# Kernel tuning notes

Hardware: AMD Instinct MI355X
Metric: run time of the kernel (lower is better)

Reference implementation:

```python
import jax, jax.numpy as jnp
import numpy as np
import random as _pyrandom

# static config (must match init_kwargs)
LAYER_NODES = 2
NUM_LEVELS = 2
KERNEL = 3
STRIDE = 2
DILATION = 3
BN_EPS = 1e-5
B, T, C = 64, 4096, 64

# ---- static interleave-index builders (replace torch per-element cat loops with one gather) ----

def _joint_indices(a_len, b_len, node_idx):
    # Block.joint: interleave a (cur) with skip=2**(node_idx-1) elems of b (prev) per a-step.
    skip = 2 ** (node_idx - 1)
    idx, cnt = [], 0
    for i in range(a_len):
        for _ in range(skip):
            if cnt >= b_len:
                break
            idx.append(a_len + cnt)
            cnt += 1
        idx.append(i)
    return np.asarray(idx, np.int32)


def _joint_explict_indices(a_len, b_len, c_len):
    # Block.joint_explict: round-robin a,b,c then tails in order a,b,c.
    m = min(a_len, b_len, c_len)
    idx = []
    for t in range(m):
        idx += [t, a_len + t, a_len + b_len + t]
    idx += list(range(m, a_len))
    idx += list(range(a_len + m, a_len + b_len))
    idx += list(range(a_len + b_len + m, a_len + b_len + c_len))
    return np.asarray(idx, np.int32)


def _dpadding_indices(a_len, num_padding):
    # Block.dpadding: duplicate every skip_cnt-th element until num_padding extras inserted.
    if num_padding == 0:
        return np.arange(a_len, dtype=np.int32)
    target = a_len + num_padding
    skip_cnt = a_len // num_padding
    mult = None
    if skip_cnt == 0:
        mult = num_padding // a_len
        skip_cnt = 1
    entries = []  # list-of-lists mimics torch list entries (slab counts as 1 entry, as in source)
    rem = num_padding
    for i in range(a_len):
        if rem == 0:
            entries.append(list(range(i, a_len)))
            break
        if i % skip_cnt == 0:
            entries.append([i])
            rem -= 1
        if mult is not None:
            entries.extend([[i]] * mult)
        entries.append([i])
    if len(entries) > target:  # randrange pop path; deterministic seed (never hit for these shapes)
        rng = _pyrandom.Random(0)
        for _ in range(len(entries) - target):
            entries.pop(rng.randrange(len(entries)))
    return np.asarray([k for e in entries for k in e], np.int32)


def _sew_up_indices(a_len, b_len, cur_layer, sp, st):
    # Block.sew_up for cur_layer > 0; st carries the mutable skip_* counters.
    idx = []
    cnt_a = cnt_b = 0
    while cnt_a < a_len:
        if sp:
            break
        if cnt_a == 0:
            pv = cnt_b  # prev_val captured once in torch source
            for _ in range(st['skip_p']):
                idx.append(a_len + pv)
                cnt_b += 1
            if cur_layer % 2 != 0:
                idx.append(0)
                cnt_a += 1
            if cnt_a == 0:
                cnt_a = 1
            continue
        for _ in range(st['skip_n']):
            if cnt_b >= b_len:
                break
            idx.append(a_len + cnt_b)
            cnt_b += 1
        if not st['skip_t']:
            for _ in range(st['skip_s']):
                if cnt_b >= b_len:
                    break
                idx.append(a_len + cnt_b)
                cnt_b += 1
                st['skip_t'] = True
        else:
            for _j in range(st['skip_d']):
                for _i in range(st['skip_s']):
                    if cnt_b >= b_len:
                        break
                    idx.append(a_len + cnt_b)
                    cnt_b += 1
                if cnt_a >= a_len:
                    break
                idx.append(cnt_a)
                cnt_a += 1
                st['skip_t'] = False
            continue
        idx.append(cnt_a)
        cnt_a += 1
    idx += [a_len + j for j in range(cnt_b, b_len)]
    if sp:
        idx += list(range(cnt_a, a_len))
    st['skip_s'] += 1
    st['skip_n'] = 3 * st['skip_n'] + st['skip_s'] + st['skip_d'] * st['skip_s']
    if cur_layer % 2 != 0:
        st['skip_p'] += 1
    return np.asarray(idx, np.int32)

# ---- jax compute blocks ----

def _conv_block(y, v, g, b):
    # weight_norm(Conv1d): w = g * v / ||v||_(in,k) per out-channel; then MaxPool1d(3,2,pad=1), ELU (dropout=0)
    nrm = jnp.sqrt(jnp.sum(v * v, axis=(1, 2), keepdims=True))
    w = (g[:, None, None] / nrm) * v
    y = jax.lax.conv_general_dilated(y, w, (STRIDE,), 'VALID', rhs_dilation=(DILATION,),
                                     dimension_numbers=('NCH', 'OIH', 'NCH'))
    y = y + b[None, :, None]
    y = jax.lax.reduce_window(y, -jnp.inf, jax.lax.max, (1, 1, KERNEL), (1, 1, STRIDE),
                              ((0, 0), (0, 0), (1, 1)))
    return jax.nn.elu(y)


def _batchnorm(y, gamma, beta):
    # BatchNorm1d training-mode batch stats (biased var), per channel over (N, L)
    mu = jnp.mean(y, axis=(0, 2), keepdims=True)
    var = jnp.mean((y - mu) ** 2, axis=(0, 2), keepdims=True)
    return gamma[None, :, None] * (y - mu) * jax.lax.rsqrt(var + BN_EPS) + beta[None, :, None]


def _communicate(xn, prev_out, node_idx, mean, std, conv_v, conv_g, conv_b, bn_gamma, bn_beta):
    if node_idx == 0:
        return xn
    while prev_out.shape[2] != xn.shape[2]:  # static-shape loop
        prev_out = jnp.diff(prev_out, axis=2)
    out_mean = 0.8 * xn / mean + 0.2 * prev_out
    out_std = 0.8 * xn / std + 0.2 * prev_out
    L = xn.shape[2]
    je = _joint_explict_indices(L, L, L)
    joined = jnp.concatenate([out_mean, prev_out, out_std], axis=2)[:, :, je]
    y = jnp.exp(_conv_block(joined, conv_v, conv_g, conv_b) ** 2 / -2)
    pad_idx = _dpadding_indices(y.shape[2], L - y.shape[2])
    y = y[:, :, pad_idx]
    y = _batchnorm(y, bn_gamma, bn_beta)
    y = jax.nn.elu(y)  # Dropout(0.1) in eval -> identity
    return xn + y


def _forward(x, conv_v, conv_g, conv_b, bn_gamma, bn_beta):
    x = jnp.transpose(x, (0, 2, 1))  # [B, C, T]
    mean = jnp.mean(x)
    std = jnp.std(x, ddof=1)  # torch.std is unbiased
    # Graph.build_graph: level l node (l*LAYER_NODES + i) = x strided by LAYER_NODES, l+1 times
    nodes = {}
    for i in range(LAYER_NODES):
        cur = x
        for lvl in range(NUM_LEVELS):
            cur = cur[:, :, i::LAYER_NODES]
            assert cur.shape[2] >= 10, 'sp stat-padding path not exercised with these shapes'
            nodes[lvl * LAYER_NODES + i] = cur
    st = dict(skip_p=1, skip_s=1, skip_d=2, skip_n=3, skip_t=False)
    prev_layer_out = None
    cur_layer_out = None
    for i in range(NUM_LEVELS):
        cur_layer_out = None
        prev_out = None
        for j in range(LAYER_NODES + 1):
            cur_node = i * LAYER_NODES if j == LAYER_NODES else j + i * LAYER_NODES
            node_idx = j % LAYER_NODES
            out = _communicate(nodes[cur_node], prev_out, node_idx, mean, std,
                               conv_v, conv_g, conv_b, bn_gamma, bn_beta)
            prev_out = out
            if cur_layer_out is None:
                cur_layer_out = out
            if node_idx != 0:
                ji = _joint_indices(prev_out.shape[2], cur_layer_out.shape[2], node_idx)
                cur_layer_out = jnp.concatenate([prev_out, cur_layer_out], axis=2)[:, :, ji]
            if j == LAYER_NODES and i > 0:  # sew_up is identity at level 0
                si = _sew_up_indices(cur_layer_out.shape[2], prev_layer_out.shape[2], i, False, st)
                cur_layer_out = jnp.concatenate([cur_layer_out, prev_layer_out], axis=2)[:, :, si]
        prev_layer_out = cur_layer_out
    return cur_layer_out  # [B, C, 6144]


def setup_inputs() -> dict:
    key = jax.random.key(0)
    k1, k2, k3 = jax.random.split(key, 3)
    return {
        'x': jax.random.normal(k1, (B, T, C), dtype=jnp.float32),
        'conv_v': jax.random.normal(k2, (C, C, KERNEL), dtype=jnp.float32) * 0.1,
        'conv_g': jax.random.uniform(k3, (C,), dtype=jnp.float32) + 0.5,
        'conv_b': jnp.zeros((C,), jnp.float32),
        'bn_gamma': jnp.ones((C,), jnp.float32),
        'bn_beta': jnp.zeros((C,), jnp.float32),
    }


def reference(x, conv_v, conv_g, conv_b, bn_gamma, bn_beta):
    return _forward(x, conv_v, conv_g, conv_b, bn_gamma, bn_beta)
```

## Files before the change

### kernel.cpp

```cpp
#include <hip/hip_runtime.h>
#include <math.h>

#define BB 64
#define TT 4096
#define CC 64

constexpr int L0v = 2048, U0v = 3069, V0v = 1535, P0v = 2048;
constexpr int L1v = 1024, U1v = 1533, V1v = 767,  P1v = 1024;
constexpr int OUTL = 6144;
constexpr long NTOT = (long)BB * TT * CC;
#define VB 30
#define NB0 52
#define NB1 26
#define NTILE ((NB0 + NB1) * 64)
#define SRTOT 87
#define RSTR 65
#define EROWS 63

__global__ __launch_bounds__(256) void transpose_stats(const float* __restrict__ x,
                                                       float* __restrict__ xtr,
                                                       double* __restrict__ part) {
  __shared__ float tile[64][65];
  __shared__ double sd1[256], sd2[256];
  const int tt = blockIdx.x;
  const int b = blockIdx.y;
  const int t0 = tt * 64;
  const long xbase = (long)b * TT * CC + (long)t0 * CC;
  const int tid = threadIdx.x;
  double a = 0, q = 0;
  {
    int c = tid & 63;
    for (int r = tid >> 6; r < 64; r += 4) {
      float v = x[xbase + r * 64 + c];
      tile[r][c] = v;
      a += v; q += (double)v * (double)v;
    }
  }
  sd1[tid] = a; sd2[tid] = q;
  __syncthreads();
  {
    int tl = tid & 63;
    for (int cc = tid >> 6; cc < 64; cc += 4)
      xtr[((long)(b * 64 + cc)) * TT + t0 + tl] = tile[tl][cc];
  }
  for (int s = 128; s > 0; s >>= 1) {
    if (tid < s) { sd1[tid] += sd1[tid + s]; sd2[tid] += sd2[tid + s]; }
    __syncthreads();
  }
  if (tid == 0) {
    part[(b * 64 + tt) * 2] = sd1[0];
    part[(b * 64 + tt) * 2 + 1] = sd2[0];
  }
}

__device__ __host__ inline int pad_idx(int p, int brk, int dup, int sub) {
  if (p < brk) { int q = p / 3; int r = p - 3 * q; return 2 * q + (r == 2 ? 1 : 0); }
  if (p < brk + 2) return dup;
  return p - sub;
}

__device__ inline int fmap_code(int k) {
  if (k == 0) return 2048 + 0;
  if (k == 1) return 0;
  if (k < 5462) {
    int m = k - 2;
    int c = m / 12;
    int j = m - 12 * c;
    if (j <= 3)  return 2048 + (1 + 9 * c + j);
    if (j == 4)  return 1 + 3 * c;
    if (j <= 8)  return 2048 + (9 * c + j);
    if (j == 9)  return 2 + 3 * c;
    if (j == 10) return 2048 + (9 + 9 * c);
    return 3 + 3 * c;
  }
  return k - 4096;
}

__global__ __launch_bounds__(256) void prep(const double* __restrict__ part,
                                            double* __restrict__ stats,
                                            const float* __restrict__ v,
                                            const float* __restrict__ g,
                                            float* __restrict__ wt,
                                            int* __restrict__ codes) {
  const int blk = blockIdx.x;
  const int tid = threadIdx.x;
  if (blk == 0) {
    __shared__ double s1[256], s2[256];
    double a = 0, q = 0;
    for (int i = tid; i < 4096; i += 256) { a += part[2 * i]; q += part[2 * i + 1]; }
    s1[tid] = a; s2[tid] = q;
    __syncthreads();
    for (int s = 128; s > 0; s >>= 1) {
      if (tid < s) { s1[tid] += s1[tid + s]; s2[tid] += s2[tid + s]; }
      __syncthreads();
    }
    if (tid == 0) {
      double n = (double)NTOT;
      double mean = s1[0] / n;
      double var = (s2[0] - s1[0] * s1[0] / n) / (n - 1.0);
      stats[0] = mean; stats[1] = sqrt(var);
      stats[2] = 0.8 / mean;
      stats[3] = 0.8 / sqrt(var);
    }
  } else if (blk <= 64) {
    int o = blk - 1;
    __shared__ float red[256];
    __shared__ float scale;
    float vv = (tid < 192) ? v[o * 192 + tid] : 0.f;
    red[tid] = vv * vv;
    __syncthreads();
    for (int s = 128; s > 0; s >>= 1) {
      if (tid < s) red[tid] += red[tid + s];
      __syncthreads();
    }
    if (tid == 0) scale = g[o] / sqrtf(red[0]);
    __syncthreads();
    if (tid < 192) {
      int i = tid / 3, k = tid - 3 * i;
      wt[(k * 64 + i) * 64 + o] = scale * vv;
    }
  } else {
    int k = (blk - 65) * 256 + tid;
    if (k < OUTL) {
      int s = fmap_code(k);
      int type, xi, yi = 0;
      if (s < 2048) {
        if ((s & 1) == 0) { type = 0; xi = 2 * s; }
        else { int p = s >> 1; yi = pad_idx(p, 768, 512, 257); xi = 4 * p + 3; type = 2; }
      } else {
        int p = s - 2048;
        if ((p & 1) == 0) { type = 0; xi = p; }
        else { int q = p >> 1; yi = pad_idx(q, 1536, 1024, 513); xi = 2 * q + 1; type = 1; }
      }
      codes[k] = type | (xi << 2) | (yi << 14);
    }
  }
}

__global__ __launch_bounds__(256, 7) void conv_pool(
    const float* __restrict__ x, const float* __restrict__ wt,
    const float* __restrict__ cbias, const double* __restrict__ stats,
    float* __restrict__ y10, float* __restrict__ y11,
    float* __restrict__ part) {
  const int b = blockIdx.x;
  const int jb = blockIdx.y;
  const bool lev0 = jb < NB0;
  const int v0 = (lev0 ? jb : jb - NB0) * VB;
  const int L = lev0 ? L0v : L1v;
  const int U = lev0 ? U0v : U1v;
  const int V = lev0 ? V0v : V1v;
  const int mult = lev0 ? 2 : 4;
  const int off1 = lev0 ? 1 : 3;
  const int mid = lev0 ? 1024 : 512;
  float* __restrict__ y1 = lev0 ? y10 : y11;

  const int tid = threadIdx.x;
  const int lane = tid & 63;
  const int og = __builtin_amdgcn_readfirstlane((tid >> 6) * 16);

  const int a0 = (v0 == 0) ? 0 : (2 * v0 - 1) / 3;

  __shared__ __align__(16) float S[SRTOT * RSTR];
  float* cbf = S;
  float* red = S + 4096;

  const float ivm = (float)stats[2];
  const float ivs = (float)stats[3];
  const long xbase = (long)b * TT * CC;

  for (int idx = tid; idx < SRTOT * 16; idx += 256) {
    int d = idx >> 4, c4 = (idx & 15) * 4;
    int T = (d < 44) ? (2 * a0 + d) : (2 * a0 + d - 44);
    int Tc = min(max(T, 0), L - 1);
    long row = (long)(mult * Tc) * CC + ((d < 44) ? 0 : off1) * CC;
    float4 vr = *(const float4*)&x[xbase + row + c4];
    float* dst = S + d * RSTR + c4;
    dst[0] = vr.x; dst[1] = vr.y; dst[2] = vr.z; dst[3] = vr.w;
  }
  __syncthreads();

  const int rho = (lane <= 41) ? lane : ((lane == 63) ? 0 : (44 + 2 * (lane - 42)));
  const float* Sx = S + rho * RSTR;

  float acc[16];
#pragma unroll
  for (int oo = 0; oo < 16; oo++) acc[oo] = 0.f;

  for (int k = 0; k < 3; k++) {
    const float* Sk = Sx + k * RSTR;
    const float* wk = wt + (k * 64) * 64 + og;
#pragma unroll 4
    for (int i4 = 0; i4 < 16; i4++) {
      float x0 = Sk[i4 * 4 + 0];
      float x1 = Sk[i4 * 4 + 1];
      float x2 = Sk[i4 * 4 + 2];
      float x3 = Sk[i4 * 4 + 3];
      const float* wp = wk + i4 * 256;
#pragma unroll
      for (int oo = 0; oo < 16; oo++) {
        float w0 = wp[oo], w1 = wp[64 + oo], w2 = wp[128 + oo], w3 = wp[192 + oo];
        acc[oo] = fmaf(x0, w0, acc[oo]);
        acc[oo] = fmaf(x1, w1, acc[oo]);
        acc[oo] = fmaf(x2, w2, acc[oo]);
        acc[oo] = fmaf(x3, w3, acc[oo]);
      }
    }
  }

  __syncthreads();
  if (lane < EROWS) {
#pragma unroll
    for (int oo = 0; oo < 16; oo++)
      cbf[lane * RSTR + og + oo] = acc[oo];
  }
  __syncthreads();

  const int o = tid >> 2;
  const float bias = cbias[o];
  float a1 = 0.f, a2 = 0.f;
  for (int vq = tid & 3; vq < VB; vq += 4) {
    int v = v0 + vq;
    if (v < V) {
      float m3 = -INFINITY;
#pragma unroll
      for (int p = 0; p < 3; p++) {
        int u = 2 * v - 1 + p;
        float mv = -INFINITY;
        if (u >= 0 && u < U) {
          int a = u / 3;
          int r = u - 3 * a;
          int ai = a - a0;
          if (r == 2) {
            mv = cbf[(2 * ai + 1) * RSTR + o] + bias;
          } else {
            float e1 = cbf[(42 + ai) * RSTR + o];
            float e0 = cbf[(2 * ai) * RSTR + o];
            mv = fmaf(r ? ivs : ivm, e1, fmaf(0.2f, e0, bias));
          }
        }
        m3 = fmaxf(m3, mv);
      }
      float e = (m3 > 0.f) ? m3 : (expf(m3) - 1.f);
      float y = expf(-0.5f * e * e);
      y1[(long)(b * 64 + o) * V + v] = y;
      float wv = (v < mid) ? (float)(2 - (v & 1)) : ((v == mid) ? 2.f : 1.f);
      a1 += wv * y;
      a2 += wv * y * y;
    }
  }
  red[o * 4 + (tid & 3)] = a1;
  red[256 + o * 4 + (tid & 3)] = a2;
  __syncthreads();
  if (tid < 64) {
    float s1 = red[tid * 4] + red[tid * 4 + 1] + red[tid * 4 + 2] + red[tid * 4 + 3];
    float s2 = red[256 + tid * 4] + red[256 + tid * 4 + 1] + red[256 + tid * 4 + 2] + red[256 + tid * 4 + 3];
    long tile = (long)jb * 64 + b;
    part[tile * 128 + tid * 2] = s1;
    part[tile * 128 + tid * 2 + 1] = s2;
  }
}

__global__ __launch_bounds__(256) void bn_reduce(const float* __restrict__ part,
                                                 const float* __restrict__ gamma,
                                                 const float* __restrict__ beta,
                                                 float* __restrict__ cf0,
                                                 float* __restrict__ cf1) {
  const int bc = blockIdx.x;
  const int lev = bc >> 6, c = bc & 63;
  const long t_lo = lev ? (long)NB0 * 64 : 0;
  const long t_hi = lev ? (long)(NB0 + NB1) * 64 : (long)NB0 * 64;
  const int tid = threadIdx.x;
  double a = 0, q = 0;
  for (long t = t_lo + tid; t < t_hi; t += 256) {
    a += part[t * 128 + c * 2];
    q += part[t * 128 + c * 2 + 1];
  }
  __shared__ double s1[256], s2[256];
  s1[tid] = a; s2[tid] = q;
  __syncthreads();
  for (int s = 128; s > 0; s >>= 1) {
    if (tid < s) { s1[tid] += s1[tid + s]; s2[tid] += s2[tid + s]; }
    __syncthreads();
  }
  if (tid == 0) {
    double n = (double)BB * (lev ? P1v : P0v);
    double mu = s1[0] / n;
    double var = s2[0] / n - mu * mu;
    float rsig = 1.0f / sqrtf((float)var + 1e-5f);
    float A = gamma[c] * rsig;
    float Bv = beta[c] - (float)mu * A;
    float* cf = lev ? cf1 : cf0;
    cf[2 * c] = A;
    cf[2 * c + 1] = Bv;
  }
}

__global__ __launch_bounds__(256) void final_fused(
    const float* __restrict__ xtr, const float* __restrict__ y10,
    const float* __restrict__ y11, const float* __restrict__ cf0,
    const float* __restrict__ cf1, const int* __restrict__ codes,
    float* __restrict__ out) {
  const int bc = blockIdx.y;
  const int k = blockIdx.x * 256 + threadIdx.x;
  const int c = bc & 63;
  const float A0 = cf0[2 * c], B0 = cf0[2 * c + 1];
  const float A1 = cf1[2 * c], B1 = cf1[2 * c + 1];
  const float* xr  = xtr + (long)bc * TT;
  const float* y0r = y10 + (long)bc * V0v;
  const float* y1r = y11 + (long)bc * V1v;

  int code = codes[k];
  int type = code & 3;
  int xi = (code >> 2) & 4095;
  int yi = code >> 14;
  float xv = xr[xi];
  const float* yrow = (type == 2) ? y1r : y0r;
  float yv = yrow[yi];
  float A = (type == 0) ? 0.f : ((type == 2) ? A1 : A0);
  float Bv = (type == 0) ? 0.f : ((type == 2) ? B1 : B0);
  float z = fmaf(A, yv, Bv);
  float e = (z > 0.f) ? z : (expf(z) - 1.f);
  out[(long)bc * OUTL + k] = xv + e;
}

extern "C" void kernel_launch(void* const* d_in, const int* in_sizes, int n_in,
                              void* d_out, int out_size, void* d_ws, size_t ws_size,
                              hipStream_t stream) {
  const float* x   = (const float*)d_in[0];
  const float* cv  = (const float*)d_in[1];
  const float* cg  = (const float*)d_in[2];
  const float* cb  = (const float*)d_in[3];
  const float* gam = (const float*)d_in[4];
  const float* bet = (const float*)d_in[5];
  float* out = (float*)d_out;

  char* ws = (char*)d_ws;
  size_t cur = 0;
  auto alloc = [&](size_t bytes) -> char* {
    char* p = ws + cur;
    cur = (cur + bytes + 255) & ~(size_t)255;
    return p;
  };
  double* part   = (double*)alloc(4096 * 2 * sizeof(double));
  double* stats  = (double*)alloc(4 * sizeof(double));
  float*  wt     = (float*)alloc(3 * 64 * 64 * sizeof(float));
  float*  bnp    = (float*)alloc((size_t)NTILE * 128 * sizeof(float));
  float*  cf0    = (float*)alloc(128 * sizeof(float));
  float*  cf1    = (float*)alloc(128 * sizeof(float));
  int*    codes  = (int*)alloc(OUTL * sizeof(int));
  float*  xtr    = (float*)alloc((size_t)BB * CC * TT * sizeof(float));
  float*  y10    = (float*)alloc((size_t)4096 * V0v * sizeof(float));
  float*  y11    = (float*)alloc((size_t)4096 * V1v * sizeof(float));

  transpose_stats<<<dim3(64, 64), 256, 0, stream>>>(x, xtr, part);
  prep<<<89, 256, 0, stream>>>(part, stats, cv, cg, wt, codes);

  conv_pool<<<dim3(64, NB0 + NB1), 256, 0, stream>>>(x, wt, cb, stats, y10, y11, bnp);

  bn_reduce<<<128, 256, 0, stream>>>(bnp, gam, bet, cf0, cf1);

  final_fused<<<dim3(24, 4096), 256, 0, stream>>>(xtr, y10, y11, cf0, cf1, codes, out);
}
```

Before: 362.7 us.

## Vectorize transpose, use float4 conv staging, and stage rows in LDS for final gather

The transpose kernel now loads and stores float4 and replaces the shared-memory tree reduction with wavefront shuffles. The conv kernel stages input as float4 in a group-major LDS layout, so each lane reads four channels with one LDS load. The final kernel now runs one block per (b,c) row, loads the x, y0 and y1 rows into LDS, and gathers from LDS instead of global memory. This cuts scattered global reads and block count, at the cost of lower occupancy from about 25KB of LDS per block and fewer, longer blocks.

```diff
diff --git a/kernel.cpp b/kernel.cpp
--- a/kernel.cpp
+++ b/kernel.cpp
@@ -14,6 +14,7 @@
 #define NB1 26
 #define NTILE ((NB0 + NB1) * 64)
 #define SRTOT 87
+#define GSTR 89
 #define RSTR 65
 #define EROWS 63
 
@@ -21,7 +22,7 @@
                                                        float* __restrict__ xtr,
                                                        double* __restrict__ part) {
   __shared__ float tile[64][65];
-  __shared__ double sd1[256], sd2[256];
+  __shared__ double sred[8];
   const int tt = blockIdx.x;
   const int b = blockIdx.y;
   const int t0 = tt * 64;
@@ -29,27 +30,40 @@
   const int tid = threadIdx.x;
   double a = 0, q = 0;
   {
-    int c = tid & 63;
-    for (int r = tid >> 6; r < 64; r += 4) {
-      float v = x[xbase + r * 64 + c];
-      tile[r][c] = v;
-      a += v; q += (double)v * (double)v;
-    }
-  }
-  sd1[tid] = a; sd2[tid] = q;
+    const int c4 = (tid & 15) * 4;
+    const int r0 = tid >> 4;
+#pragma unroll
+    for (int rr = 0; rr < 4; rr++) {
+      int r = r0 + rr * 16;
+      float4 v = *(const float4*)&x[xbase + r * 64 + c4];
+      tile[r][c4] = v.x; tile[r][c4 + 1] = v.y;
+      tile[r][c4 + 2] = v.z; tile[r][c4 + 3] = v.w;
+      a += (double)v.x + (double)v.y + (double)v.z + (double)v.w;
+      q += (double)v.x * v.x + (double)v.y * v.y + (double)v.z * v.z + (double)v.w * v.w;
+    }
+  }
   __syncthreads();
   {
-    int tl = tid & 63;
-    for (int cc = tid >> 6; cc < 64; cc += 4)
-      xtr[((long)(b * 64 + cc)) * TT + t0 + tl] = tile[tl][cc];
-  }
-  for (int s = 128; s > 0; s >>= 1) {
-    if (tid < s) { sd1[tid] += sd1[tid + s]; sd2[tid] += sd2[tid + s]; }
-    __syncthreads();
-  }
+    const int t4 = (tid & 15) * 4;
+    const int c0 = tid >> 4;
+#pragma unroll
+    for (int cc = 0; cc < 4; cc++) {
+      int c = c0 + cc * 16;
+      float4 v;
+      v.x = tile[t4][c]; v.y = tile[t4 + 1][c];
+      v.z = tile[t4 + 2][c]; v.w = tile[t4 + 3][c];
+      *(float4*)&xtr[((long)(b * 64 + c)) * TT + t0 + t4] = v;
+    }
+  }
+  for (int off = 32; off > 0; off >>= 1) {
+    a += __shfl_down(a, off);
+    q += __shfl_down(q, off);
+  }
+  if ((tid & 63) == 0) { sred[(tid >> 6) * 2] = a; sred[(tid >> 6) * 2 + 1] = q; }
+  __syncthreads();
   if (tid == 0) {
-    part[(b * 64 + tt) * 2] = sd1[0];
-    part[(b * 64 + tt) * 2 + 1] = sd2[0];
+    part[(b * 64 + tt) * 2]     = sred[0] + sred[2] + sred[4] + sred[6];
+    part[(b * 64 + tt) * 2 + 1] = sred[1] + sred[3] + sred[5] + sred[7];
   }
 }
 
@@ -160,49 +174,43 @@
 
   const int a0 = (v0 == 0) ? 0 : (2 * v0 - 1) / 3;
 
-  __shared__ __align__(16) float S[SRTOT * RSTR];
-  float* cbf = S;
-  float* red = S + 4096;
+  __shared__ __align__(16) float4 S2[16 * GSTR];
+  float* cbf = (float*)S2;
+  float* red = (float*)S2 + 4096;
 
   const float ivm = (float)stats[2];
   const float ivs = (float)stats[3];
   const long xbase = (long)b * TT * CC;
 
   for (int idx = tid; idx < SRTOT * 16; idx += 256) {
-    int d = idx >> 4, c4 = (idx & 15) * 4;
+    int d = idx >> 4, g = idx & 15;
     int T = (d < 44) ? (2 * a0 + d) : (2 * a0 + d - 44);
     int Tc = min(max(T, 0), L - 1);
     long row = (long)(mult * Tc) * CC + ((d < 44) ? 0 : off1) * CC;
-    float4 vr = *(const float4*)&x[xbase + row + c4];
-    float* dst = S + d * RSTR + c4;
-    dst[0] = vr.x; dst[1] = vr.y; dst[2] = vr.z; dst[3] = vr.w;
+    S2[g * GSTR + d] = *(const float4*)&x[xbase + row + g * 4];
   }
   __syncthreads();
 
   const int rho = (lane <= 41) ? lane : ((lane == 63) ? 0 : (44 + 2 * (lane - 42)));
-  const float* Sx = S + rho * RSTR;
 
   float acc[16];
 #pragma unroll
   for (int oo = 0; oo < 16; oo++) acc[oo] = 0.f;
 
   for (int k = 0; k < 3; k++) {
-    const float* Sk = Sx + k * RSTR;
-    const float* wk = wt + (k * 64) * 64 + og;
+    const float4* Sk = S2 + rho + k;
+    const float* wk = wt + k * 4096 + og;
 #pragma unroll 4
     for (int i4 = 0; i4 < 16; i4++) {
-      float x0 = Sk[i4 * 4 + 0];
-      float x1 = Sk[i4 * 4 + 1];
-      float x2 = Sk[i4 * 4 + 2];
-      float x3 = Sk[i4 * 4 + 3];
+      float4 xv = Sk[i4 * GSTR];
       const float* wp = wk + i4 * 256;
 #pragma unroll
       for (int oo = 0; oo < 16; oo++) {
         float w0 = wp[oo], w1 = wp[64 + oo], w2 = wp[128 + oo], w3 = wp[192 + oo];
-        acc[oo] = fmaf(x0, w0, acc[oo]);
-        acc[oo] = fmaf(x1, w1, acc[oo]);
-        acc[oo] = fmaf(x2, w2, acc[oo]);
-        acc[oo] = fmaf(x3, w3, acc[oo]);
+        acc[oo] = fmaf(xv.x, w0, acc[oo]);
+        acc[oo] = fmaf(xv.y, w1, acc[oo]);
+        acc[oo] = fmaf(xv.z, w2, acc[oo]);
+        acc[oo] = fmaf(xv.w, w3, acc[oo]);
       }
     }
   }
@@ -300,27 +308,46 @@
     const float* __restrict__ y11, const float* __restrict__ cf0,
     const float* __restrict__ cf1, const int* __restrict__ codes,
     float* __restrict__ out) {
-  const int bc = blockIdx.y;
-  const int k = blockIdx.x * 256 + threadIdx.x;
+  const int bc = blockIdx.x;
   const int c = bc & 63;
+  const int tid = threadIdx.x;
+  __shared__ float xs[4096];
+  __shared__ float y0s[1536];
+  __shared__ float y1s[768];
+
+  const float* xr = xtr + (long)bc * TT;
+  for (int i = tid; i < 1024; i += 256)
+    *(float4*)&xs[i * 4] = *(const float4*)&xr[i * 4];
+  const float* y0r = y10 + (long)bc * V0v;
+  for (int i = tid; i < 384; i += 256) {
+    if (i < 383) *(float4*)&y0s[i * 4] = *(const float4*)&y0r[i * 4];
+    else { y0s[1532] = y0r[1532]; y0s[1533] = y0r[1533]; y0s[1534] = y0r[1534]; }
+  }
+  const float* y1r = y11 + (long)bc * V1v;
+  for (int i = tid; i < 192; i += 256) {
+    if (i < 191) *(float4*)&y1s[i * 4] = *(const float4*)&y1r[i * 4];
+    else { y1s[764] = y1r[764]; y1s[765] = y1r[765]; y1s[766] = y1r[766]; }
+  }
+  __syncthreads();
+
   const float A0 = cf0[2 * c], B0 = cf0[2 * c + 1];
   const float A1 = cf1[2 * c], B1 = cf1[2 * c + 1];
-  const float* xr  = xtr + (long)bc * TT;
-  const float* y0r = y10 + (long)bc * V0v;
-  const float* y1r = y11 + (long)bc * V1v;
-
-  int code = codes[k];
-  int type = code & 3;
-  int xi = (code >> 2) & 4095;
-  int yi = code >> 14;
-  float xv = xr[xi];
-  const float* yrow = (type == 2) ? y1r : y0r;
-  float yv = yrow[yi];
-  float A = (type == 0) ? 0.f : ((type == 2) ? A1 : A0);
-  float Bv = (type == 0) ? 0.f : ((type == 2) ? B1 : B0);
-  float z = fmaf(A, yv, Bv);
-  float e = (z > 0.f) ? z : (expf(z) - 1.f);
-  out[(long)bc * OUTL + k] = xv + e;
+  float* orow = out + (long)bc * OUTL;
+#pragma unroll 4
+  for (int i = 0; i < 24; i++) {
+    int k = i * 256 + tid;
+    int code = codes[k];
+    int type = code & 3;
+    int xi = (code >> 2) & 4095;
+    int yi = code >> 14;
+    float xv = xs[xi];
+    float yv = (type == 2) ? y1s[yi] : y0s[yi];
+    float A = (type == 0) ? 0.f : ((type == 2) ? A1 : A0);
+    float Bv = (type == 0) ? 0.f : ((type == 2) ? B1 : B0);
+    float z = fmaf(A, yv, Bv);
+    float e = (z > 0.f) ? z : (expf(z) - 1.f);
+    orow[k] = xv + e;
+  }
 }
 
 extern "C" void kernel_launch(void* const* d_in, const int* in_sizes, int n_in,
@@ -359,5 +386,5 @@
 
   bn_reduce<<<128, 256, 0, stream>>>(bnp, gam, bet, cf0, cf1);
 
-  final_fused<<<dim3(24, 4096), 256, 0, stream>>>(xtr, y10, y11, cf0, cf1, codes, out);
-}
+  final_fused<<<4096, 256, 0, stream>>>(xtr, y10, y11, cf0, cf1, codes, out);
+}
```

Result: faster. 316.9 us (-12.6%).
